# Optimization experiments

Hardware: AMD Instinct MI355X
Metric: run time of the kernel (lower is better)

Reference implementation:

```python
import jax, jax.numpy as jnp
import numpy as np

DIM = 3072      # model dim (Qwen-Image)
HEADS = 24
HD = 128        # head dim; inner = HEADS*HD = 3072
INNER = HEADS * HD
FF = 4 * DIM    # 12288
S_IMG = 1024
S_TXT = 256
S_TOT = S_IMG + S_TXT
B = 1
EPS = 1e-6
SCALE_SHIFT = 1.0


def setup_inputs() -> dict:
    key = jax.random.key(0)
    ks = iter(jax.random.split(key, 64))
    W = 0.02

    def nrm(shape, s=W):
        return jax.random.normal(next(ks), shape, dtype=jnp.float32) * s

    # RoPE tables for the joint (txt first, then img) sequence, interleaved layout
    pos = jnp.arange(S_TOT, dtype=jnp.float32)
    inv = 1.0 / (10000.0 ** (jnp.arange(HD // 2, dtype=jnp.float32) / (HD // 2)))
    ang = pos[:, None] * inv[None, :]                       # [S, HD/2]
    rope_cos = jnp.repeat(jnp.cos(ang), 2, axis=-1)         # [S, HD]
    rope_sin = jnp.repeat(jnp.sin(ang), 2, axis=-1)

    inp = {
        "hidden_states": jax.random.normal(next(ks), (B, S_IMG, DIM), dtype=jnp.float32),
        "encoder_hidden_states": jax.random.normal(next(ks), (B, S_TXT, DIM), dtype=jnp.float32),
        "temb": jax.random.normal(next(ks), (B, DIM), dtype=jnp.float32),
        "rope_cos": rope_cos,
        "rope_sin": rope_sin,
        # modulation (AWQW4A16Linear equivalent)
        "img_mod_w": nrm((6 * DIM, DIM)), "img_mod_b": nrm((6 * DIM,)),
        "txt_mod_w": nrm((6 * DIM, DIM)), "txt_mod_b": nrm((6 * DIM,)),
        # attention (SVDQW4A4Linear equivalents)
        "qkv_w": nrm((3 * INNER, DIM)), "qkv_b": nrm((3 * INNER,)),
        "add_qkv_w": nrm((3 * INNER, DIM)), "add_qkv_b": nrm((3 * INNER,)),
        "norm_q_g": jnp.ones((HD,), jnp.float32), "norm_k_g": jnp.ones((HD,), jnp.float32),
        "norm_added_q_g": jnp.ones((HD,), jnp.float32), "norm_added_k_g": jnp.ones((HD,), jnp.float32),
        "to_out_w": nrm((DIM, INNER)), "to_out_b": nrm((DIM,)),
        "to_add_out_w": nrm((DIM, INNER)), "to_add_out_b": nrm((DIM,)),
        # MLPs
        "img_mlp_w1": nrm((FF, DIM)), "img_mlp_b1": nrm((FF,)),
        "img_mlp_w2": nrm((DIM, FF)), "img_mlp_b2": nrm((DIM,)),
        "txt_mlp_w1": nrm((FF, DIM)), "txt_mlp_b1": nrm((FF,)),
        "txt_mlp_w2": nrm((DIM, FF)), "txt_mlp_b2": nrm((DIM,)),
    }
    return inp


def _lin(x, w, b):
    return jnp.matmul(x, w.T) + b


def _ln(x):  # LayerNorm, no affine, eps=1e-6
    mu = jnp.mean(x, axis=-1, keepdims=True)
    var = jnp.mean(jnp.square(x - mu), axis=-1, keepdims=True)
    return (x - mu) * jax.lax.rsqrt(var + EPS)


def _rms(x, g):  # per-head RMSNorm over last dim (HD)
    ms = jnp.mean(jnp.square(x), axis=-1, keepdims=True)
    return x * jax.lax.rsqrt(ms + EPS) * g


def _rope(x, cos, sin):  # x: [B,S,H,D], cos/sin: [S,D], interleaved rotate
    x1 = x[..., 0::2]
    x2 = x[..., 1::2]
    xr = jnp.stack([-x2, x1], axis=-1).reshape(x.shape)
    return x * cos[None, :, None, :] + xr * sin[None, :, None, :]


def _reorder_mod(m):
    # view(B,-1,6).transpose(1,2).reshape(B,-1): de-interleave 6 modulation vecs
    b = m.shape[0]
    return m.reshape(b, DIM, 6).transpose(0, 2, 1).reshape(b, 6 * DIM)


def _modulate(x, mod):
    shift, scale, gate = jnp.split(mod, 3, axis=-1)
    return x * (scale + SCALE_SHIFT)[:, None, :] + shift[:, None, :], gate[:, None, :]


def _mlp(x, w1, b1, w2, b2):  # GELU(tanh) MLP
    h = jax.nn.gelu(_lin(x, w1, b1), approximate=True)
    return _lin(h, w2, b2)


def reference(hidden_states, encoder_hidden_states, temb, rope_cos, rope_sin,
              img_mod_w, img_mod_b, txt_mod_w, txt_mod_b,
              qkv_w, qkv_b, add_qkv_w, add_qkv_b,
              norm_q_g, norm_k_g, norm_added_q_g, norm_added_k_g,
              to_out_w, to_out_b, to_add_out_w, to_add_out_b,
              img_mlp_w1, img_mlp_b1, img_mlp_w2, img_mlp_b2,
              txt_mlp_w1, txt_mlp_b1, txt_mlp_w2, txt_mlp_b2):
    b = hidden_states.shape[0]

    img_mod = _reorder_mod(_lin(jax.nn.silu(temb), img_mod_w, img_mod_b))
    txt_mod = _reorder_mod(_lin(jax.nn.silu(temb), txt_mod_w, txt_mod_b))
    img_mod1, img_mod2 = jnp.split(img_mod, 2, axis=-1)
    txt_mod1, txt_mod2 = jnp.split(txt_mod, 2, axis=-1)

    img_modulated, img_gate1 = _modulate(_ln(hidden_states), img_mod1)
    txt_modulated, txt_gate1 = _modulate(_ln(encoder_hidden_states), txt_mod1)

    # ---- joint attention ----
    img_q, img_k, img_v = jnp.split(_lin(img_modulated, qkv_w, qkv_b), 3, axis=-1)
    txt_q, txt_k, txt_v = jnp.split(_lin(txt_modulated, add_qkv_w, add_qkv_b), 3, axis=-1)

    def heads(x):  # [B,S,INNER] -> [B,S,H,HD]
        return x.reshape(b, x.shape[1], HEADS, HD)

    img_q = _rms(heads(img_q), norm_q_g)
    img_k = _rms(heads(img_k), norm_k_g)
    txt_q = _rms(heads(txt_q), norm_added_q_g)
    txt_k = _rms(heads(txt_k), norm_added_k_g)

    q = jnp.concatenate([txt_q, img_q], axis=1)  # txt first
    k = jnp.concatenate([txt_k, img_k], axis=1)
    v = jnp.concatenate([heads(txt_v), heads(img_v)], axis=1)

    q = _rope(q, rope_cos, rope_sin)
    k = _rope(k, rope_cos, rope_sin)

    scale = 1.0 / jnp.sqrt(jnp.float32(HD))
    scores = jnp.einsum('bqhd,bkhd->bhqk', q, k) * scale
    probs = jax.nn.softmax(scores, axis=-1)
    attn = jnp.einsum('bhqk,bkhd->bqhd', probs, v).reshape(b, S_TOT, INNER)

    txt_attn = attn[:, :S_TXT, :]
    img_attn = attn[:, S_TXT:, :]
    img_attn = _lin(img_attn, to_out_w, to_out_b)
    txt_attn = _lin(txt_attn, to_add_out_w, to_add_out_b)

    hidden_states = hidden_states + img_gate1 * img_attn
    encoder_hidden_states = encoder_hidden_states + txt_gate1 * txt_attn

    # ---- MLPs ----
    img_m2, img_gate2 = _modulate(_ln(hidden_states), img_mod2)
    hidden_states = hidden_states + img_gate2 * _mlp(img_m2, img_mlp_w1, img_mlp_b1, img_mlp_w2, img_mlp_b2)

    txt_m2, txt_gate2 = _modulate(_ln(encoder_hidden_states), txt_mod2)
    encoder_hidden_states = encoder_hidden_states + txt_gate2 * _mlp(txt_m2, txt_mlp_w1, txt_mlp_b1, txt_mlp_w2, txt_mlp_b2)

    return (encoder_hidden_states, hidden_states)
```

## Files before the change

kernel.cpp:

```cpp
#include <hip/hip_runtime.h>

#define DIMC   3072
#define HEADS  24
#define HD     128
#define FF     12288
#define S_IMG  1024
#define S_TXT  256
#define S_TOT  1280
#define EPSF   1e-6f

typedef __attribute__((ext_vector_type(8))) short bf16x8;
typedef __attribute__((ext_vector_type(4))) float f32x4;
typedef __attribute__((ext_vector_type(4))) float float4v;

__device__ __forceinline__ unsigned short f2bf(float f) {
    union { float f; unsigned u; } c; c.f = f;
    unsigned u = c.u;
    unsigned r = (u + 0x7fffu + ((u >> 16) & 1u)) >> 16;
    return (unsigned short)r;
}
__device__ __forceinline__ float b2f(unsigned short h) {
    union { unsigned u; float f; } c; c.u = ((unsigned)h) << 16;
    return c.f;
}

struct GemmArgs {
    const unsigned short* A;
    const void* B;
    const float* bias;
    void* out;
    const float* base;
    const float* gate;
};

template<int EPI, bool BF16B>
__global__ __launch_bounds__(256)
void gemm_bt(GemmArgs g0, GemmArgs g1, int ysplit,
             int K, int lda, int ldb, int ldout,
             long batchA, long batchB, long batchOut)
{
    __shared__ __align__(16) unsigned short As[2][128 * 64];
    __shared__ __align__(16) unsigned short Bs[2][128 * 64];

    const int tid  = threadIdx.x;
    const int lane = tid & 63;
    const int wave = tid >> 6;
    const int wm = wave >> 1, wc = wave & 1;

    const int by = blockIdx.y;
    const bool second = (by >= ysplit);
    const GemmArgs g = second ? g1 : g0;
    const int bm = (second ? by - ysplit : by) * 128;
    const int bn = blockIdx.x * 128;

    const unsigned short* A = g.A + (long)blockIdx.z * batchA;
    const float* Bf = (const float*)g.B + (long)blockIdx.z * batchB;
    const unsigned short* Bh = (const unsigned short*)g.B + (long)blockIdx.z * batchB;

    const int kc = tid & 7;
    const int rbase = tid >> 3;

    f32x4 acc[4][4] = {};

    bf16x8  ra[4];
    bf16x8  rbh[4];
    float4v rb0[4], rb1[4];

    auto LOAD = [&](int t) {
        long kof = (long)t * 64 + kc * 8;
        #pragma unroll
        for (int i = 0; i < 4; i++) {
            int r = i * 32 + rbase;
            ra[i] = *(const bf16x8*)(A + (long)(bm + r) * lda + kof);
            if constexpr (BF16B) {
                rbh[i] = *(const bf16x8*)(Bh + (long)(bn + r) * ldb + kof);
            } else {
                const float* src = Bf + (long)(bn + r) * ldb + kof;
                rb0[i] = *(const float4v*)src;
                rb1[i] = *(const float4v*)(src + 4);
            }
        }
    };

    auto STORE = [&](int buf) {
        #pragma unroll
        for (int i = 0; i < 4; i++) {
            int r = i * 32 + rbase;
            int off = r * 128 + ((kc * 16) ^ ((r & 7) << 4));
            *(bf16x8*)((char*)As[buf] + off) = ra[i];
            bf16x8 v;
            if constexpr (BF16B) {
                v = rbh[i];
            } else {
                v[0] = (short)f2bf(rb0[i][0]); v[1] = (short)f2bf(rb0[i][1]);
                v[2] = (short)f2bf(rb0[i][2]); v[3] = (short)f2bf(rb0[i][3]);
                v[4] = (short)f2bf(rb1[i][0]); v[5] = (short)f2bf(rb1[i][1]);
                v[6] = (short)f2bf(rb1[i][2]); v[7] = (short)f2bf(rb1[i][3]);
            }
            *(bf16x8*)((char*)Bs[buf] + off) = v;
        }
    };

    auto COMPUTE = [&](int buf) {
        #pragma unroll
        for (int ks = 0; ks < 2; ks++) {
            const int kb = ks * 64 + (lane >> 4) * 16;
            bf16x8 af[4], bfr[4];
            #pragma unroll
            for (int mi = 0; mi < 4; mi++) {
                int r = wm * 64 + mi * 16 + (lane & 15);
                af[mi] = *(const bf16x8*)((const char*)As[buf] + r * 128 + (kb ^ ((r & 7) << 4)));
            }
            #pragma unroll
            for (int ni = 0; ni < 4; ni++) {
                int r = wc * 64 + ni * 16 + (lane & 15);
                bfr[ni] = *(const bf16x8*)((const char*)Bs[buf] + r * 128 + (kb ^ ((r & 7) << 4)));
            }
            #pragma unroll
            for (int mi = 0; mi < 4; mi++)
                #pragma unroll
                for (int ni = 0; ni < 4; ni++)
                    acc[mi][ni] = __builtin_amdgcn_mfma_f32_16x16x32_bf16(
                        af[mi], bfr[ni], acc[mi][ni], 0, 0, 0);
        }
    };

    const int nk = K >> 6;
    LOAD(0);
    STORE(0);
    __syncthreads();
    for (int t = 0; t < nk; ++t) {
        const int cur = t & 1;
        if (t + 1 < nk) LOAD(t + 1);
        COMPUTE(cur);
        if (t + 1 < nk) STORE(cur ^ 1);
        __syncthreads();
    }

    unsigned short* outh = (unsigned short*)g.out + (long)blockIdx.z * batchOut;
    float*          outf = (float*)g.out + (long)blockIdx.z * batchOut;
    #pragma unroll
    for (int mi = 0; mi < 4; mi++) {
        #pragma unroll
        for (int ni = 0; ni < 4; ni++) {
            int n = bn + wc * 64 + ni * 16 + (lane & 15);
            float bv = g.bias ? g.bias[n] : 0.0f;
            #pragma unroll
            for (int r = 0; r < 4; r++) {
                int m = bm + wm * 64 + mi * 16 + (lane >> 4) * 4 + r;
                float v = acc[mi][ni][r] + bv;
                long o = (long)m * ldout + n;
                if constexpr (EPI == 0) {
                    outf[o] = v;
                } else if constexpr (EPI == 1) {
                    outh[o] = f2bf(v);
                } else if constexpr (EPI == 2) {
                    float t = tanhf(0.7978845608028654f * (v + 0.044715f * v * v * v));
                    outh[o] = f2bf(0.5f * v * (1.0f + t));
                } else {
                    outf[o] = g.base[o] + g.gate[n] * v;
                }
            }
        }
    }
}

__global__ void silu_k(const float* __restrict__ x, float* __restrict__ out) {
    int i = blockIdx.x * 256 + threadIdx.x;
    if (i < DIMC) { float v = x[i]; out[i] = v / (1.0f + expf(-v)); }
}

__global__ __launch_bounds__(256)
void mod_gemv(const float* __restrict__ st,
              const float* __restrict__ Wimg, const float* __restrict__ bimg,
              const float* __restrict__ Wtxt, const float* __restrict__ btxt,
              float* __restrict__ mimg, float* __restrict__ mtxt)
{
    int wv = threadIdx.x >> 6, lane = threadIdx.x & 63;
    int r = blockIdx.x * 4 + wv;
    const float* W = blockIdx.y ? Wtxt : Wimg;
    const float* b = blockIdx.y ? btxt : bimg;
    float* out = blockIdx.y ? mtxt : mimg;
    const float* row = W + (long)r * DIMC;
    float acc = 0.f;
    #pragma unroll
    for (int j = 0; j < 12; j++) {
        float4v wvv = ((const float4v*)row)[lane + j * 64];
        float4v xv  = ((const float4v*)st)[lane + j * 64];
        acc += wvv[0] * xv[0] + wvv[1] * xv[1] + wvv[2] * xv[2] + wvv[3] * xv[3];
    }
    #pragma unroll
    for (int o = 32; o; o >>= 1) acc += __shfl_xor(acc, o);
    if (lane == 0) {
        int d = r / 6, j6 = r % 6;
        out[j6 * DIMC + d] = acc + b[r];
    }
}

__global__ __launch_bounds__(256)
void ln_mod(const float* __restrict__ x, const float* __restrict__ shift,
            const float* __restrict__ scale, unsigned short* __restrict__ out)
{
    __shared__ float red[8];
    long row = blockIdx.x;
    const float* xr = x + row * DIMC;
    float4v v[3];
    float sum = 0.f, sq = 0.f;
    #pragma unroll
    for (int j = 0; j < 3; j++) {
        v[j] = ((const float4v*)xr)[threadIdx.x + j * 256];
        #pragma unroll
        for (int c = 0; c < 4; c++) { sum += v[j][c]; sq += v[j][c] * v[j][c]; }
    }
    int lane = threadIdx.x & 63, wv = threadIdx.x >> 6;
    #pragma unroll
    for (int o = 32; o; o >>= 1) { sum += __shfl_xor(sum, o); sq += __shfl_xor(sq, o); }
    if (lane == 0) { red[wv] = sum; red[4 + wv] = sq; }
    __syncthreads();
    sum = red[0] + red[1] + red[2] + red[3];
    sq  = red[4] + red[5] + red[6] + red[7];
    float mu = sum / DIMC;
    float var = sq / DIMC - mu * mu;
    float rstd = rsqrtf(var + EPSF);
    #pragma unroll
    for (int j = 0; j < 3; j++) {
        int nb = (threadIdx.x + j * 256) * 4;
        #pragma unroll
        for (int c = 0; c < 4; c++) {
            int n = nb + c;
            float y = (v[j][c] - mu) * rstd * (scale[n] + 1.0f) + shift[n];
            out[row * DIMC + n] = f2bf(y);
        }
    }
}

__global__ __launch_bounds__(64)
void qkv_post(const float* __restrict__ qkv_img, const float* __restrict__ qkv_txt,
              const float* __restrict__ nqg, const float* __restrict__ nkg,
              const float* __restrict__ naqg, const float* __restrict__ nakg,
              const float* __restrict__ rc, const float* __restrict__ rs,
              unsigned short* __restrict__ q, unsigned short* __restrict__ k,
              unsigned short* __restrict__ vt)
{
    int s = blockIdx.x;
    int h = blockIdx.y;
    int d0 = threadIdx.x;
    const float *src, *gq, *gk;
    if (s < S_TXT) { src = qkv_txt + (long)s * 3 * DIMC; gq = naqg; gk = nakg; }
    else           { src = qkv_img + (long)(s - S_TXT) * 3 * DIMC; gq = nqg; gk = nkg; }

    float q0 = src[h * HD + d0],            q1 = src[h * HD + d0 + 64];
    float k0 = src[DIMC + h * HD + d0],     k1 = src[DIMC + h * HD + d0 + 64];
    float v0 = src[2 * DIMC + h * HD + d0], v1 = src[2 * DIMC + h * HD + d0 + 64];

    float sqq = q0 * q0 + q1 * q1;
    float sqk = k0 * k0 + k1 * k1;
    #pragma unroll
    for (int o = 32; o; o >>= 1) { sqq += __shfl_xor(sqq, o); sqk += __shfl_xor(sqk, o); }
    float rq = rsqrtf(sqq / (float)HD + EPSF);
    float rk = rsqrtf(sqk / (float)HD + EPSF);
    q0 *= rq * gq[d0]; q1 *= rq * gq[d0 + 64];
    k0 *= rk * gk[d0]; k1 *= rk * gk[d0 + 64];

    float qp0 = __shfl_xor(q0, 1), qp1 = __shfl_xor(q1, 1);
    float kp0 = __shfl_xor(k0, 1), kp1 = __shfl_xor(k1, 1);
    float c0 = rc[(long)s * HD + d0], c1 = rc[(long)s * HD + d0 + 64];
    float s0 = rs[(long)s * HD + d0], s1 = rs[(long)s * HD + d0 + 64];
    float sgn = (d0 & 1) ? 1.0f : -1.0f;
    float qo0 = q0 * c0 + sgn * qp0 * s0;
    float qo1 = q1 * c1 + sgn * qp1 * s1;
    float ko0 = k0 * c0 + sgn * kp0 * s0;
    float ko1 = k1 * c1 + sgn * kp1 * s1;

    const float scl = 0.08838834764831845f;
    long qkbase = ((long)h * S_TOT + s) * HD;
    q[qkbase + d0]      = f2bf(qo0 * scl);
    q[qkbase + d0 + 64] = f2bf(qo1 * scl);
    k[qkbase + d0]      = f2bf(ko0);
    k[qkbase + d0 + 64] = f2bf(ko1);
    vt[((long)h * HD + d0) * S_TOT + s]        = f2bf(v0);
    vt[((long)h * HD + d0 + 64) * S_TOT + s]   = f2bf(v1);
}

__global__ __launch_bounds__(256)
void softmax_k(unsigned short* __restrict__ scores)
{
    long row = (long)blockIdx.x * 4 + (threadIdx.x >> 6);
    int lane = threadIdx.x & 63;
    unsigned short* p = scores + row * S_TOT;
    float v[20];
    float mx = -1e30f;
    #pragma unroll
    for (int j = 0; j < 20; j++) { v[j] = b2f(p[lane + j * 64]); mx = fmaxf(mx, v[j]); }
    #pragma unroll
    for (int o = 32; o; o >>= 1) mx = fmaxf(mx, __shfl_xor(mx, o));
    float sum = 0.f;
    #pragma unroll
    for (int j = 0; j < 20; j++) { v[j] = expf(v[j] - mx); sum += v[j]; }
    #pragma unroll
    for (int o = 32; o; o >>= 1) sum += __shfl_xor(sum, o);
    float inv = 1.0f / sum;
    #pragma unroll
    for (int j = 0; j < 20; j++) p[lane + j * 64] = f2bf(v[j] * inv);
}

extern "C" void kernel_launch(void* const* d_in, const int* in_sizes, int n_in,
                              void* d_out, int out_size, void* d_ws, size_t ws_size,
                              hipStream_t stream)
{
    const float* hidden   = (const float*)d_in[0];
    const float* enc      = (const float*)d_in[1];
    const float* temb     = (const float*)d_in[2];
    const float* rope_cos = (const float*)d_in[3];
    const float* rope_sin = (const float*)d_in[4];
    const float* img_mod_w = (const float*)d_in[5];
    const float* img_mod_b = (const float*)d_in[6];
    const float* txt_mod_w = (const float*)d_in[7];
    const float* txt_mod_b = (const float*)d_in[8];
    const float* qkv_w     = (const float*)d_in[9];
    const float* qkv_b     = (const float*)d_in[10];
    const float* add_qkv_w = (const float*)d_in[11];
    const float* add_qkv_b = (const float*)d_in[12];
    const float* norm_q_g  = (const float*)d_in[13];
    const float* norm_k_g  = (const float*)d_in[14];
    const float* norm_aq_g = (const float*)d_in[15];
    const float* norm_ak_g = (const float*)d_in[16];
    const float* to_out_w  = (const float*)d_in[17];
    const float* to_out_b  = (const float*)d_in[18];
    const float* to_add_out_w = (const float*)d_in[19];
    const float* to_add_out_b = (const float*)d_in[20];
    const float* img_mlp_w1 = (const float*)d_in[21];
    const float* img_mlp_b1 = (const float*)d_in[22];
    const float* img_mlp_w2 = (const float*)d_in[23];
    const float* img_mlp_b2 = (const float*)d_in[24];
    const float* txt_mlp_w1 = (const float*)d_in[25];
    const float* txt_mlp_b1 = (const float*)d_in[26];
    const float* txt_mlp_w2 = (const float*)d_in[27];
    const float* txt_mlp_b2 = (const float*)d_in[28];

    char* w = (char*)d_ws;
    auto alloc = [&](size_t bytes) { char* p = w; w += (bytes + 255) & ~(size_t)255; return p; };
    float* silu_t  = (float*)alloc(DIMC * 4);
    float* mod_img = (float*)alloc(6 * DIMC * 4);
    float* mod_txt = (float*)alloc(6 * DIMC * 4);
    unsigned short* mA_img = (unsigned short*)alloc((long)S_IMG * DIMC * 2);
    unsigned short* mA_txt = (unsigned short*)alloc((long)S_TXT * DIMC * 2);
    float* qkv_img = (float*)alloc((long)S_IMG * 3 * DIMC * 4);
    float* qkv_txt = (float*)alloc((long)S_TXT * 3 * DIMC * 4);
    unsigned short* qb = (unsigned short*)alloc((long)HEADS * S_TOT * HD * 2);
    unsigned short* kb = (unsigned short*)alloc((long)HEADS * S_TOT * HD * 2);
    unsigned short* vt = (unsigned short*)alloc((long)HEADS * HD * S_TOT * 2);
    unsigned short* scores = (unsigned short*)alloc((long)HEADS * S_TOT * S_TOT * 2);
    unsigned short* attn = (unsigned short*)alloc((long)S_TOT * DIMC * 2);
    float* h1_img = (float*)alloc((long)S_IMG * DIMC * 4);
    float* h1_txt = (float*)alloc((long)S_TXT * DIMC * 4);
    unsigned short* gelu_img = (unsigned short*)alloc((long)S_IMG * FF * 2);
    unsigned short* gelu_txt = (unsigned short*)alloc((long)S_TXT * FF * 2);

    float* out_enc = (float*)d_out;
    float* out_hid = (float*)d_out + (long)S_TXT * DIMC;

    silu_k<<<12, 256, 0, stream>>>(temb, silu_t);
    mod_gemv<<<dim3(4608, 2), 256, 0, stream>>>(silu_t, img_mod_w, img_mod_b,
                                                txt_mod_w, txt_mod_b, mod_img, mod_txt);

    ln_mod<<<S_IMG, 256, 0, stream>>>(hidden, mod_img, mod_img + DIMC, mA_img);
    ln_mod<<<S_TXT, 256, 0, stream>>>(enc, mod_txt, mod_txt + DIMC, mA_txt);

    {
        GemmArgs gi{mA_img, qkv_w, qkv_b, qkv_img, nullptr, nullptr};
        GemmArgs gt{mA_txt, add_qkv_w, add_qkv_b, qkv_txt, nullptr, nullptr};
        gemm_bt<0, false><<<dim3(72, 10, 1), 256, 0, stream>>>(
            gi, gt, 8, DIMC, DIMC, DIMC, 3 * DIMC, 0, 0, 0);
    }

    qkv_post<<<dim3(S_TOT, HEADS), 64, 0, stream>>>(
        qkv_img, qkv_txt, norm_q_g, norm_k_g, norm_aq_g, norm_ak_g,
        rope_cos, rope_sin, qb, kb, vt);

    {
        GemmArgs gs{qb, kb, nullptr, scores, nullptr, nullptr};
        gemm_bt<1, true><<<dim3(10, 10, HEADS), 256, 0, stream>>>(
            gs, gs, 10, HD, HD, HD, S_TOT,
            (long)S_TOT * HD, (long)S_TOT * HD, (long)S_TOT * S_TOT);
    }
    softmax_k<<<(HEADS * S_TOT) / 4, 256, 0, stream>>>(scores);
    {
        GemmArgs gp{scores, vt, nullptr, attn, nullptr, nullptr};
        gemm_bt<1, true><<<dim3(1, 10, HEADS), 256, 0, stream>>>(
            gp, gp, 10, S_TOT, S_TOT, S_TOT, DIMC,
            (long)S_TOT * S_TOT, (long)HD * S_TOT, HD);
    }

    {
        GemmArgs gi{attn + (long)S_TXT * DIMC, to_out_w, to_out_b, h1_img, hidden, mod_img + 2 * DIMC};
        GemmArgs gt{attn, to_add_out_w, to_add_out_b, h1_txt, enc, mod_txt + 2 * DIMC};
        gemm_bt<3, false><<<dim3(24, 10, 1), 256, 0, stream>>>(
            gi, gt, 8, DIMC, DIMC, DIMC, DIMC, 0, 0, 0);
    }

    ln_mod<<<S_IMG, 256, 0, stream>>>(h1_img, mod_img + 3 * DIMC, mod_img + 4 * DIMC, mA_img);
    ln_mod<<<S_TXT, 256, 0, stream>>>(h1_txt, mod_txt + 3 * DIMC, mod_txt + 4 * DIMC, mA_txt);

    {
        GemmArgs gi{mA_img, img_mlp_w1, img_mlp_b1, gelu_img, nullptr, nullptr};
        GemmArgs gt{mA_txt, txt_mlp_w1, txt_mlp_b1, gelu_txt, nullptr, nullptr};
        gemm_bt<2, false><<<dim3(96, 10, 1), 256, 0, stream>>>(
            gi, gt, 8, DIMC, DIMC, DIMC, FF, 0, 0, 0);
    }
    {
        GemmArgs gi{gelu_img, img_mlp_w2, img_mlp_b2, out_hid, h1_img, mod_img + 5 * DIMC};
        GemmArgs gt{gelu_txt, txt_mlp_w2, txt_mlp_b2, out_enc, h1_txt, mod_txt + 5 * DIMC};
        gemm_bt<3, false><<<dim3(24, 10, 1), 256, 0, stream>>>(
            gi, gt, 8, FF, FF, FF, DIMC, 0, 0, 0);
    }
}
```

Measured before the change: 927.2 us.

## Stage GEMM tiles via direct global-to-LDS loads, convert fp32 weights at fragment read

Replaces the register-staged global load plus LDS store with global_load_lds (16-byte direct-to-LDS) for both A and B tiles, keeping the XOR swizzle. For fp32 weights the raw fp32 tile now goes into LDS, which doubles B's shared memory footprint, and the bf16 conversion moves into the per-fragment read inside the compute loop. The aim is to cut VGPR pressure and the instruction overhead of staging. The costs are more LDS traffic and capacity, possible lower occupancy, and conversion work repeated on every fragment read. The loop relies on __syncthreads alone to order the asynchronous LDS writes with no explicit vmcnt wait, which may be unsafe.

```diff
diff --git a/kernel.cpp b/kernel.cpp
--- a/kernel.cpp
+++ b/kernel.cpp
@@ -24,6 +24,11 @@
     return c.f;
 }
 
+#define GLL16(gsrc, ldst)                                                     \
+    __builtin_amdgcn_global_load_lds(                                         \
+        (const __attribute__((address_space(1))) void*)(gsrc),                \
+        (__attribute__((address_space(3))) void*)(ldst), 16, 0, 0)
+
 struct GemmArgs {
     const unsigned short* A;
     const void* B;
@@ -39,8 +44,11 @@
              int K, int lda, int ldb, int ldout,
              long batchA, long batchB, long batchOut)
 {
-    __shared__ __align__(16) unsigned short As[2][128 * 64];
-    __shared__ __align__(16) unsigned short Bs[2][128 * 64];
+    constexpr int ASZ = 128 * 64 * 2;
+    constexpr int BSZ = BF16B ? 128 * 64 * 2 : 128 * 64 * 4;
+    __shared__ __align__(16) char smem[2 * ASZ + 2 * BSZ];
+    char* smemA = smem;
+    char* smemB = smem + 2 * ASZ;
 
     const int tid  = threadIdx.x;
     const int lane = tid & 63;
@@ -57,64 +65,72 @@
     const float* Bf = (const float*)g.B + (long)blockIdx.z * batchB;
     const unsigned short* Bh = (const unsigned short*)g.B + (long)blockIdx.z * batchB;
 
-    const int kc = tid & 7;
-    const int rbase = tid >> 3;
-
-    f32x4 acc[4][4] = {};
-
-    bf16x8  ra[4];
-    bf16x8  rbh[4];
-    float4v rb0[4], rb1[4];
-
-    auto LOAD = [&](int t) {
-        long kof = (long)t * 64 + kc * 8;
+    const int rA_lane = (lane >> 3);
+    const int cA = (lane & 7) ^ (rA_lane & 7);
+    const int rB_lane = (lane >> 4);
+    const int rB7 = (wave * 4 + rB_lane) & 7;
+    const int cBf = (lane & 15) ^ (rB7 << 1);
+
+    auto STAGE = [&](int buf, int t) {
+        const long kof = (long)t * 64;
         #pragma unroll
         for (int i = 0; i < 4; i++) {
-            int r = i * 32 + rbase;
-            ra[i] = *(const bf16x8*)(A + (long)(bm + r) * lda + kof);
-            if constexpr (BF16B) {
-                rbh[i] = *(const bf16x8*)(Bh + (long)(bn + r) * ldb + kof);
-            } else {
-                const float* src = Bf + (long)(bn + r) * ldb + kof;
-                rb0[i] = *(const float4v*)src;
-                rb1[i] = *(const float4v*)(src + 4);
+            int r = i * 32 + wave * 8 + rA_lane;
+            GLL16(A + (long)(bm + r) * lda + kof + cA * 8,
+                  smemA + buf * ASZ + i * 4096 + wave * 1024);
+        }
+        if constexpr (BF16B) {
+            #pragma unroll
+            for (int i = 0; i < 4; i++) {
+                int r = i * 32 + wave * 8 + rA_lane;
+                GLL16(Bh + (long)(bn + r) * ldb + kof + cA * 8,
+                      smemB + buf * BSZ + i * 4096 + wave * 1024);
+            }
+        } else {
+            #pragma unroll
+            for (int i = 0; i < 8; i++) {
+                int r = i * 16 + wave * 4 + rB_lane;
+                GLL16(Bf + (long)(bn + r) * ldb + kof + cBf * 4,
+                      smemB + buf * BSZ + i * 4096 + wave * 1024);
             }
         }
     };
 
-    auto STORE = [&](int buf) {
-        #pragma unroll
-        for (int i = 0; i < 4; i++) {
-            int r = i * 32 + rbase;
-            int off = r * 128 + ((kc * 16) ^ ((r & 7) << 4));
-            *(bf16x8*)((char*)As[buf] + off) = ra[i];
-            bf16x8 v;
-            if constexpr (BF16B) {
-                v = rbh[i];
-            } else {
-                v[0] = (short)f2bf(rb0[i][0]); v[1] = (short)f2bf(rb0[i][1]);
-                v[2] = (short)f2bf(rb0[i][2]); v[3] = (short)f2bf(rb0[i][3]);
-                v[4] = (short)f2bf(rb1[i][0]); v[5] = (short)f2bf(rb1[i][1]);
-                v[6] = (short)f2bf(rb1[i][2]); v[7] = (short)f2bf(rb1[i][3]);
-            }
-            *(bf16x8*)((char*)Bs[buf] + off) = v;
-        }
-    };
+    f32x4 acc[4][4] = {};
+    const int sA = (lane & 7) << 4;
+    const int sB32 = (lane & 7) << 5;
 
     auto COMPUTE = [&](int buf) {
         #pragma unroll
         for (int ks = 0; ks < 2; ks++) {
-            const int kb = ks * 64 + (lane >> 4) * 16;
+            const int kbA = ks * 64 + (lane >> 4) * 16;
             bf16x8 af[4], bfr[4];
             #pragma unroll
             for (int mi = 0; mi < 4; mi++) {
                 int r = wm * 64 + mi * 16 + (lane & 15);
-                af[mi] = *(const bf16x8*)((const char*)As[buf] + r * 128 + (kb ^ ((r & 7) << 4)));
+                af[mi] = *(const bf16x8*)(smemA + buf * ASZ + r * 128 + (kbA ^ sA));
             }
-            #pragma unroll
-            for (int ni = 0; ni < 4; ni++) {
-                int r = wc * 64 + ni * 16 + (lane & 15);
-                bfr[ni] = *(const bf16x8*)((const char*)Bs[buf] + r * 128 + (kb ^ ((r & 7) << 4)));
+            if constexpr (BF16B) {
+                #pragma unroll
+                for (int ni = 0; ni < 4; ni++) {
+                    int r = wc * 64 + ni * 16 + (lane & 15);
+                    bfr[ni] = *(const bf16x8*)(smemB + buf * BSZ + r * 128 + (kbA ^ sA));
+                }
+            } else {
+                const int kbB = ks * 128 + (lane >> 4) * 32;
+                #pragma unroll
+                for (int ni = 0; ni < 4; ni++) {
+                    int r = wc * 64 + ni * 16 + (lane & 15);
+                    const char* p = smemB + buf * BSZ + r * 256 + (kbB ^ sB32);
+                    float4v b0 = *(const float4v*)p;
+                    float4v b1 = *(const float4v*)(p + 16);
+                    bf16x8 v;
+                    v[0] = (short)f2bf(b0[0]); v[1] = (short)f2bf(b0[1]);
+                    v[2] = (short)f2bf(b0[2]); v[3] = (short)f2bf(b0[3]);
+                    v[4] = (short)f2bf(b1[0]); v[5] = (short)f2bf(b1[1]);
+                    v[6] = (short)f2bf(b1[2]); v[7] = (short)f2bf(b1[3]);
+                    bfr[ni] = v;
+                }
             }
             #pragma unroll
             for (int mi = 0; mi < 4; mi++)
@@ -126,14 +142,11 @@
     };
 
     const int nk = K >> 6;
-    LOAD(0);
-    STORE(0);
+    STAGE(0, 0);
     __syncthreads();
     for (int t = 0; t < nk; ++t) {
-        const int cur = t & 1;
-        if (t + 1 < nk) LOAD(t + 1);
-        COMPUTE(cur);
-        if (t + 1 < nk) STORE(cur ^ 1);
+        if (t + 1 < nk) STAGE((t + 1) & 1, t + 1);
+        COMPUTE(t & 1);
         __syncthreads();
     }
 
```

Result: slower. 1.055 ms (+13.8%).
